# Performance work log

Hardware: AMD Instinct MI355X
Metric: run time of the kernel (lower is better)

## Reference

```python
import jax, jax.numpy as jnp
import numpy as np

N = 100000
D = 256
E = 300000


def setup_inputs() -> dict:
    key = jax.random.key(0)
    ks = jax.random.split(key, 9)
    x_all = jax.random.normal(ks[0], (N, D), dtype=jnp.float32)
    edge_index = jax.random.randint(ks[1], (2, E), 0, N, dtype=jnp.int64)
    s = 1.0 / np.sqrt(D)
    params = {}
    for i, layer in enumerate(["1", "2", "3"]):
        params[f"Wl{layer}"] = jax.random.uniform(ks[2 + 2 * i], (D, D), jnp.float32, -s, s)
        params[f"Wr{layer}"] = jax.random.uniform(ks[3 + 2 * i], (D, D), jnp.float32, -s, s)
        params[f"b{layer}"] = jnp.zeros((D,), jnp.float32)
    return {"edge_index": edge_index, "x_all": x_all, **params}


def sage_conv(x, src, dst, Wl, Wr, b):
    # PyG SAGEConv: lin_l(mean_{j in N(i)} x_j) + lin_r(x_i), bias on lin_l
    msgs = x[src]                                        # [E, D] gather
    agg = jax.ops.segment_sum(msgs, dst, num_segments=N)  # [N, D]
    deg = jax.ops.segment_sum(jnp.ones((src.shape[0],), x.dtype), dst, num_segments=N)
    agg = agg / jnp.maximum(deg, 1.0)[:, None]           # mean; isolated nodes -> 0
    return agg @ Wl.T + x @ Wr.T + b


def reference(edge_index, x_all, Wl1, Wr1, b1, Wl2, Wr2, b2, Wl3, Wr3, b3):
    src, dst = edge_index[0], edge_index[1]
    x = jax.nn.relu(sage_conv(x_all, src, dst, Wl1, Wr1, b1))
    # dropout p=0.4 is identity at inference (training=False)
    x = jax.nn.relu(sage_conv(x, src, dst, Wl2, Wr2, b2))
    x = sage_conv(x, src, dst, Wl3, Wr3, b3)
    return x
```

## Files before the change

### kernel.cpp

```cpp
#include <hip/hip_runtime.h>

typedef unsigned short ushort_t;
typedef __attribute__((ext_vector_type(8))) short bf16x8;
typedef __attribute__((ext_vector_type(4))) float f32x4;

#define NNODES 100000
#define DIM    256
#define NEDGE  300000
#define KTOT   512
#define KSTEPS 16
#define BROWS  128
#define NTILES 16
#define SLICE  16384


__global__ void count_kernel(const int* __restrict__ dst, int* __restrict__ cnt, int E) {
    int e = blockIdx.x * blockDim.x + threadIdx.x;
    if (e < E) atomicAdd(&cnt[dst[e]], 1);
}

__global__ void scan1(const int* __restrict__ cnt, int* __restrict__ partial, int n) {
    __shared__ int s[256];
    int i = blockIdx.x * 256 + threadIdx.x;
    s[threadIdx.x] = (i < n) ? cnt[i] : 0;
    __syncthreads();
    for (int off = 128; off > 0; off >>= 1) {
        if (threadIdx.x < off) s[threadIdx.x] += s[threadIdx.x + off];
        __syncthreads();
    }
    if (threadIdx.x == 0) partial[blockIdx.x] = s[0];
}

__global__ void scan2(int* __restrict__ partial, int nb) {
    __shared__ int s[512];
    int t = threadIdx.x;
    int orig = (t < nb) ? partial[t] : 0;
    s[t] = orig;
    __syncthreads();
    for (int off = 1; off < 512; off <<= 1) {
        int v = (t >= off) ? s[t - off] : 0;
        __syncthreads();
        s[t] += v;
        __syncthreads();
    }
    if (t < nb) partial[t] = s[t] - orig;
}

__global__ void scan3(const int* __restrict__ cnt, const int* __restrict__ partial,
                      int* __restrict__ row_start, int n) {
    __shared__ int s[256];
    int i = blockIdx.x * 256 + threadIdx.x;
    int v = (i < n) ? cnt[i] : 0;
    s[threadIdx.x] = v;
    __syncthreads();
    for (int off = 1; off < 256; off <<= 1) {
        int t = (threadIdx.x >= off) ? s[threadIdx.x - off] : 0;
        __syncthreads();
        s[threadIdx.x] += t;
        __syncthreads();
    }
    if (i < n) row_start[i] = partial[blockIdx.x] + s[threadIdx.x] - v;
}

__global__ void fill_csr(const int* __restrict__ src, const int* __restrict__ dst,
                         const int* __restrict__ row_start, int* __restrict__ cursor,
                         int* __restrict__ esrc, int E) {
    int e = blockIdx.x * blockDim.x + threadIdx.x;
    if (e < E) {
        int d = dst[e];
        int pos = row_start[d] + atomicAdd(&cursor[d], 1);
        esrc[pos] = src[e];
    }
}

__global__ __launch_bounds__(256) void aggregate(
    const int* __restrict__ esrc, const int* __restrict__ row_start,
    const int* __restrict__ cnt, const float* __restrict__ x, float* __restrict__ agg)
{
    int node = (blockIdx.x * blockDim.x + threadIdx.x) >> 6;
    int lane = threadIdx.x & 63;
    if (node >= NNODES) return;
    int start = row_start[node];
    int c = cnt[node];
    float4 acc = make_float4(0.f, 0.f, 0.f, 0.f);
    for (int i = 0; i < c; i++) {
        int s = esrc[start + i];
        float4 v = ((const float4*)(x + (size_t)s * DIM))[lane];
        acc.x += v.x; acc.y += v.y; acc.z += v.z; acc.w += v.w;
    }
    float inv = (c > 0) ? 1.0f / (float)c : 0.0f;
    ((float4*)(agg + (size_t)node * DIM))[lane] =
        make_float4(acc.x * inv, acc.y * inv, acc.z * inv, acc.w * inv);
}

__global__ void conv_weights(const float* __restrict__ Wl, const float* __restrict__ Wr,
                             ushort_t* __restrict__ Bsw) {
    int idx = blockIdx.x * 256 + threadIdx.x;
    if (idx >= 256 * KTOT) return;
    int n = idx >> 9, k = idx & 511;
    float v = (k < DIM) ? Wl[n * DIM + k] : Wr[n * DIM + (k - DIM)];
    unsigned u = __float_as_uint(v);
    unsigned hb = u & 0xFFFF0000u;
    float lo = v - __uint_as_float(hb);
    int ks = k >> 5, q = (k >> 3) & 3, j = k & 7;
    int ct = n >> 4, nn = n & 15;
    int base = ks * SLICE + ct * 512 + q * 128 + nn * 8 + j;
    Bsw[base]        = (ushort_t)(u >> 16);
    Bsw[base + 8192] = (ushort_t)(__float_as_uint(lo) >> 16);
}


__device__ __forceinline__ void stage_b(const ushort_t* __restrict__ slice,
                                        ushort_t* buf, int tid) {
    #pragma unroll
    for (int i = 0; i < 8; i++) {
        int c = tid + i * 256;
        *(bf16x8*)(buf + c * 8) = *(const bf16x8*)(slice + c * 8);
    }
}

__device__ __forceinline__ void load_a(const float* __restrict__ base, int row0, int row1,
                                       int kk, int M, float* va ) {
    if (row0 < M) {
        *(float4*)(va + 0) = *(const float4*)(base + (size_t)row0 * DIM + kk);
        *(float4*)(va + 4) = *(const float4*)(base + (size_t)row0 * DIM + kk + 4);
    } else {
        *(float4*)(va + 0) = make_float4(0.f, 0.f, 0.f, 0.f);
        *(float4*)(va + 4) = make_float4(0.f, 0.f, 0.f, 0.f);
    }
    if (row1 < M) {
        *(float4*)(va + 8)  = *(const float4*)(base + (size_t)row1 * DIM + kk);
        *(float4*)(va + 12) = *(const float4*)(base + (size_t)row1 * DIM + kk + 4);
    } else {
        *(float4*)(va + 8)  = make_float4(0.f, 0.f, 0.f, 0.f);
        *(float4*)(va + 12) = make_float4(0.f, 0.f, 0.f, 0.f);
    }
}

__device__ __forceinline__ void split8(const float* __restrict__ a, bf16x8& h, bf16x8& l) {
    #pragma unroll
    for (int i = 0; i < 8; i++) {
        float x = a[i];
        unsigned u = __float_as_uint(x);
        unsigned hb = u & 0xFFFF0000u;
        h[i] = (short)(u >> 16);
        float lo = x - __uint_as_float(hb);
        l[i] = (short)(__float_as_uint(lo) >> 16);
    }
}

__global__ __launch_bounds__(256, 2) void sage_gemm_mfma(
    const float* __restrict__ agg, const float* __restrict__ xin,
    const ushort_t* __restrict__ Bsw,
    const float* __restrict__ bias, float* __restrict__ out, int M, int do_relu)
{
    __shared__ __align__(16) ushort_t Bs[2][SLICE];

    const int tid  = threadIdx.x;
    const int lane = tid & 63;
    const int wave = tid >> 6;
    const int lrow = lane & 15;
    const int quad = lane >> 4;

    const int rowbase = blockIdx.x * BROWS + wave * 32;
    const int arow0 = rowbase + lrow;
    const int arow1 = rowbase + 16 + lrow;
    const int kq    = quad * 8;
    const int fragoff = quad * 128 + lrow * 8;

    f32x4 acc[2][NTILES];
    #pragma unroll
    for (int i = 0; i < 2; i++)
        #pragma unroll
        for (int j = 0; j < NTILES; j++)
            acc[i][j] = (f32x4){0.f, 0.f, 0.f, 0.f};

    float aC[16], aN[16];
    stage_b(Bsw, &Bs[0][0], tid);
    load_a(agg, arow0, arow1, kq, M, aC);

    for (int ks = 0; ks < KSTEPS; ks++) {
        __syncthreads();
        if (ks + 1 < KSTEPS) {
            int ks1 = ks + 1;
            stage_b(Bsw + ks1 * SLICE, &Bs[ks1 & 1][0], tid);
            const float* base = (ks1 < 8) ? agg : xin;
            int kk = ((ks1 < 8) ? ks1 * 32 : (ks1 - 8) * 32) + kq;
            load_a(base, arow0, arow1, kk, M, aN);
        }

        bf16x8 ah0, al0, ah1, al1;
        split8(aC + 0, ah0, al0);
        split8(aC + 8, ah1, al1);

        const ushort_t* bp = &Bs[ks & 1][0];
        #pragma unroll
        for (int ct = 0; ct < NTILES; ct++) {
            const bf16x8 bh = *(const bf16x8*)(bp + ct * 512 + fragoff);
            const bf16x8 bl = *(const bf16x8*)(bp + 8192 + ct * 512 + fragoff);
            acc[0][ct] = __builtin_amdgcn_mfma_f32_16x16x32_bf16(ah0, bh, acc[0][ct], 0, 0, 0);
            acc[1][ct] = __builtin_amdgcn_mfma_f32_16x16x32_bf16(ah1, bh, acc[1][ct], 0, 0, 0);
            acc[0][ct] = __builtin_amdgcn_mfma_f32_16x16x32_bf16(al0, bh, acc[0][ct], 0, 0, 0);
            acc[1][ct] = __builtin_amdgcn_mfma_f32_16x16x32_bf16(al1, bh, acc[1][ct], 0, 0, 0);
            acc[0][ct] = __builtin_amdgcn_mfma_f32_16x16x32_bf16(ah0, bl, acc[0][ct], 0, 0, 0);
            acc[1][ct] = __builtin_amdgcn_mfma_f32_16x16x32_bf16(ah1, bl, acc[1][ct], 0, 0, 0);
        }

        if (ks + 1 < KSTEPS) {
            #pragma unroll
            for (int i = 0; i < 16; i++) aC[i] = aN[i];
        }
    }

    #pragma unroll
    for (int ct = 0; ct < NTILES; ct++) {
        const int col = ct * 16 + lrow;
        const float bv = bias[col];
        #pragma unroll
        for (int rt = 0; rt < 2; rt++) {
            const int row = rowbase + rt * 16 + quad * 4;
            #pragma unroll
            for (int r = 0; r < 4; r++) {
                if (row + r < M) {
                    float v = acc[rt][ct][r] + bv;
                    if (do_relu) v = fmaxf(v, 0.f);
                    out[(size_t)(row + r) * DIM + col] = v;
                }
            }
        }
    }
}

extern "C" void kernel_launch(void* const* d_in, const int* in_sizes, int n_in,
                              void* d_out, int out_size, void* d_ws, size_t ws_size,
                              hipStream_t stream) {
    const int*   edge = (const int*)d_in[0];
    const int*   src  = edge;
    const int*   dst  = edge + NEDGE;
    const float* x    = (const float*)d_in[1];
    const float* Wl1  = (const float*)d_in[2];
    const float* Wr1  = (const float*)d_in[3];
    const float* b1   = (const float*)d_in[4];
    const float* Wl2  = (const float*)d_in[5];
    const float* Wr2  = (const float*)d_in[6];
    const float* b2   = (const float*)d_in[7];
    const float* Wl3  = (const float*)d_in[8];
    const float* Wr3  = (const float*)d_in[9];
    const float* b3   = (const float*)d_in[10];

    const size_t feat = (size_t)NNODES * DIM;
    float*    agg       = (float*)d_ws;
    float*    h2        = agg + feat;
    int*      cnt       = (int*)(h2 + feat);
    int*      row_start = cnt + NNODES;
    int*      cursor    = row_start + NNODES;
    int*      partial   = cursor + NNODES;
    int*      esrc      = partial + 512;
    ushort_t* Bsw       = (ushort_t*)(esrc + NEDGE);
    float*    h1        = (float*)d_out;

    const int nScanBlocks = (NNODES + 255) / 256;

    hipMemsetAsync(cnt, 0, NNODES * sizeof(int), stream);
    hipMemsetAsync(cursor, 0, NNODES * sizeof(int), stream);
    count_kernel<<<(NEDGE + 255) / 256, 256, 0, stream>>>(dst, cnt, NEDGE);
    scan1<<<nScanBlocks, 256, 0, stream>>>(cnt, partial, NNODES);
    scan2<<<1, 512, 0, stream>>>(partial, nScanBlocks);
    scan3<<<nScanBlocks, 256, 0, stream>>>(cnt, partial, row_start, NNODES);
    fill_csr<<<(NEDGE + 255) / 256, 256, 0, stream>>>(src, dst, row_start, cursor, esrc, NEDGE);

    const int aggBlocks  = (NNODES * 64 + 255) / 256;
    const int gemmBlocks = (NNODES + BROWS - 1) / BROWS;
    const int convBlocks = (256 * KTOT + 255) / 256;

    conv_weights<<<convBlocks, 256, 0, stream>>>(Wl1, Wr1, Bsw);
    aggregate<<<aggBlocks, 256, 0, stream>>>(esrc, row_start, cnt, x, agg);
    sage_gemm_mfma<<<gemmBlocks, 256, 0, stream>>>(agg, x, Bsw, b1, h1, NNODES, 1);

    conv_weights<<<convBlocks, 256, 0, stream>>>(Wl2, Wr2, Bsw);
    aggregate<<<aggBlocks, 256, 0, stream>>>(esrc, row_start, cnt, h1, agg);
    sage_gemm_mfma<<<gemmBlocks, 256, 0, stream>>>(agg, h1, Bsw, b2, h2, NNODES, 1);

    conv_weights<<<convBlocks, 256, 0, stream>>>(Wl3, Wr3, Bsw);
    aggregate<<<aggBlocks, 256, 0, stream>>>(esrc, row_start, cnt, h2, agg);
    sage_gemm_mfma<<<gemmBlocks, 256, 0, stream>>>(agg, h2, Bsw, b3, (float*)d_out, NNODES, 0);
}
```

Measured before the change: 620.9 us.

## Stage GEMM weights asynchronously into LDS and split columns across eight waves

Weight slices are now copied straight from global memory into LDS with global_load_lds instead of passing through registers. The GEMM block grows to 512 threads (8 waves): waves are arranged as 4 row groups by 2 column groups, each holding half the accumulator tiles, which cuts register pressure and adds waves per CU. The A-operand prefetch is reordered so the split happens before the next load is issued, with no separate copy buffer. The trade-off is that each A row is now loaded by two waves, doubling A traffic from cache.

```diff
diff --git a/kernel.cpp b/kernel.cpp
--- a/kernel.cpp
+++ b/kernel.cpp
@@ -1,6 +1,7 @@
 #include <hip/hip_runtime.h>
 
 typedef unsigned short ushort_t;
+typedef unsigned int   u32;
 typedef __attribute__((ext_vector_type(8))) short bf16x8;
 typedef __attribute__((ext_vector_type(4))) float f32x4;
 
@@ -11,6 +12,7 @@
 #define KSTEPS 16
 #define BROWS  128
 #define NTILES 16
+#define WCT    8
 #define SLICE  16384
 
 
@@ -110,12 +112,17 @@
 }
 
 
-__device__ __forceinline__ void stage_b(const ushort_t* __restrict__ slice,
-                                        ushort_t* buf, int tid) {
-    #pragma unroll
-    for (int i = 0; i < 8; i++) {
-        int c = tid + i * 256;
-        *(bf16x8*)(buf + c * 8) = *(const bf16x8*)(slice + c * 8);
+__device__ __forceinline__ void stage_b_async(const ushort_t* __restrict__ slice,
+                                              ushort_t* buf, int tid) {
+    const int wave = tid >> 6;
+    #pragma unroll
+    for (int i = 0; i < 4; i++) {
+        const int c  = tid + i * 512;
+        const int cb = wave * 64 + i * 512;
+        __builtin_amdgcn_global_load_lds(
+            (const __attribute__((address_space(1))) u32*)(slice + (size_t)c * 8),
+            (__attribute__((address_space(3))) u32*)(buf + cb * 8),
+            16, 0, 0);
     }
 }
 
@@ -149,7 +156,7 @@
     }
 }
 
-__global__ __launch_bounds__(256, 2) void sage_gemm_mfma(
+__global__ __launch_bounds__(512, 4) void sage_gemm_mfma(
     const float* __restrict__ agg, const float* __restrict__ xin,
     const ushort_t* __restrict__ Bsw,
     const float* __restrict__ bias, float* __restrict__ out, int M, int do_relu)
@@ -161,60 +168,59 @@
     const int wave = tid >> 6;
     const int lrow = lane & 15;
     const int quad = lane >> 4;
-
-    const int rowbase = blockIdx.x * BROWS + wave * 32;
+    const int rg   = wave >> 1;
+    const int cg   = wave & 1;
+
+    const int rowbase = blockIdx.x * BROWS + rg * 32;
     const int arow0 = rowbase + lrow;
     const int arow1 = rowbase + 16 + lrow;
     const int kq    = quad * 8;
-    const int fragoff = quad * 128 + lrow * 8;
-
-    f32x4 acc[2][NTILES];
+    const int ctbase = cg * WCT;
+
+    f32x4 acc[2][WCT];
     #pragma unroll
     for (int i = 0; i < 2; i++)
         #pragma unroll
-        for (int j = 0; j < NTILES; j++)
+        for (int j = 0; j < WCT; j++)
             acc[i][j] = (f32x4){0.f, 0.f, 0.f, 0.f};
 
-    float aC[16], aN[16];
-    stage_b(Bsw, &Bs[0][0], tid);
-    load_a(agg, arow0, arow1, kq, M, aC);
+    float aN[16];
+    stage_b_async(Bsw, &Bs[0][0], tid);
+    load_a(agg, arow0, arow1, kq, M, aN);
 
     for (int ks = 0; ks < KSTEPS; ks++) {
         __syncthreads();
+        if (ks + 1 < KSTEPS)
+            stage_b_async(Bsw + (size_t)(ks + 1) * SLICE, &Bs[(ks + 1) & 1][0], tid);
+
+        bf16x8 ah0, al0, ah1, al1;
+        split8(aN + 0, ah0, al0);
+        split8(aN + 8, ah1, al1);
+
         if (ks + 1 < KSTEPS) {
             int ks1 = ks + 1;
-            stage_b(Bsw + ks1 * SLICE, &Bs[ks1 & 1][0], tid);
             const float* base = (ks1 < 8) ? agg : xin;
             int kk = ((ks1 < 8) ? ks1 * 32 : (ks1 - 8) * 32) + kq;
             load_a(base, arow0, arow1, kk, M, aN);
         }
 
-        bf16x8 ah0, al0, ah1, al1;
-        split8(aC + 0, ah0, al0);
-        split8(aC + 8, ah1, al1);
-
-        const ushort_t* bp = &Bs[ks & 1][0];
+        const ushort_t* bp = &Bs[ks & 1][ctbase * 512 + lane * 8];
         #pragma unroll
-        for (int ct = 0; ct < NTILES; ct++) {
-            const bf16x8 bh = *(const bf16x8*)(bp + ct * 512 + fragoff);
-            const bf16x8 bl = *(const bf16x8*)(bp + 8192 + ct * 512 + fragoff);
-            acc[0][ct] = __builtin_amdgcn_mfma_f32_16x16x32_bf16(ah0, bh, acc[0][ct], 0, 0, 0);
-            acc[1][ct] = __builtin_amdgcn_mfma_f32_16x16x32_bf16(ah1, bh, acc[1][ct], 0, 0, 0);
-            acc[0][ct] = __builtin_amdgcn_mfma_f32_16x16x32_bf16(al0, bh, acc[0][ct], 0, 0, 0);
-            acc[1][ct] = __builtin_amdgcn_mfma_f32_16x16x32_bf16(al1, bh, acc[1][ct], 0, 0, 0);
-            acc[0][ct] = __builtin_amdgcn_mfma_f32_16x16x32_bf16(ah0, bl, acc[0][ct], 0, 0, 0);
-            acc[1][ct] = __builtin_amdgcn_mfma_f32_16x16x32_bf16(ah1, bl, acc[1][ct], 0, 0, 0);
+        for (int j = 0; j < WCT; j++) {
+            const bf16x8 bh = *(const bf16x8*)(bp + j * 512);
+            const bf16x8 bl = *(const bf16x8*)(bp + 8192 + j * 512);
+            acc[0][j] = __builtin_amdgcn_mfma_f32_16x16x32_bf16(ah0, bh, acc[0][j], 0, 0, 0);
+            acc[1][j] = __builtin_amdgcn_mfma_f32_16x16x32_bf16(ah1, bh, acc[1][j], 0, 0, 0);
+            acc[0][j] = __builtin_amdgcn_mfma_f32_16x16x32_bf16(al0, bh, acc[0][j], 0, 0, 0);
+            acc[1][j] = __builtin_amdgcn_mfma_f32_16x16x32_bf16(al1, bh, acc[1][j], 0, 0, 0);
+            acc[0][j] = __builtin_amdgcn_mfma_f32_16x16x32_bf16(ah0, bl, acc[0][j], 0, 0, 0);
+            acc[1][j] = __builtin_amdgcn_mfma_f32_16x16x32_bf16(ah1, bl, acc[1][j], 0, 0, 0);
         }
-
-        if (ks + 1 < KSTEPS) {
-            #pragma unroll
-            for (int i = 0; i < 16; i++) aC[i] = aN[i];
-        }
-    }
-
-    #pragma unroll
-    for (int ct = 0; ct < NTILES; ct++) {
-        const int col = ct * 16 + lrow;
+    }
+
+    #pragma unroll
+    for (int j = 0; j < WCT; j++) {
+        const int col = (ctbase + j) * 16 + lrow;
         const float bv = bias[col];
         #pragma unroll
         for (int rt = 0; rt < 2; rt++) {
@@ -222,7 +228,7 @@
             #pragma unroll
             for (int r = 0; r < 4; r++) {
                 if (row + r < M) {
-                    float v = acc[rt][ct][r] + bv;
+                    float v = acc[rt][j][r] + bv;
                     if (do_relu) v = fmaxf(v, 0.f);
                     out[(size_t)(row + r) * DIM + col] = v;
                 }
@@ -275,13 +281,13 @@
 
     conv_weights<<<convBlocks, 256, 0, stream>>>(Wl1, Wr1, Bsw);
     aggregate<<<aggBlocks, 256, 0, stream>>>(esrc, row_start, cnt, x, agg);
-    sage_gemm_mfma<<<gemmBlocks, 256, 0, stream>>>(agg, x, Bsw, b1, h1, NNODES, 1);
+    sage_gemm_mfma<<<gemmBlocks, 512, 0, stream>>>(agg, x, Bsw, b1, h1, NNODES, 1);
 
     conv_weights<<<convBlocks, 256, 0, stream>>>(Wl2, Wr2, Bsw);
     aggregate<<<aggBlocks, 256, 0, stream>>>(esrc, row_start, cnt, h1, agg);
-    sage_gemm_mfma<<<gemmBlocks, 256, 0, stream>>>(agg, h1, Bsw, b2, h2, NNODES, 1);
+    sage_gemm_mfma<<<gemmBlocks, 512, 0, stream>>>(agg, h1, Bsw, b2, h2, NNODES, 1);
 
     conv_weights<<<convBlocks, 256, 0, stream>>>(Wl3, Wr3, Bsw);
     aggregate<<<aggBlocks, 256, 0, stream>>>(esrc, row_start, cnt, h2, agg);
-    sage_gemm_mfma<<<gemmBlocks, 256, 0, stream>>>(agg, h2, Bsw, b3, (float*)d_out, NNODES, 0);
-}
+    sage_gemm_mfma<<<gemmBlocks, 512, 0, stream>>>(agg, h2, Bsw, b3, (float*)d_out, NNODES, 0);
+}
```

New measurement: 615.4 us. No clear change (-0.9%).
